# Optimization experiments

Hardware: AMD Instinct MI355X
Metric: run time of the kernel (lower is better)

Reference implementation:

```python
import jax, jax.numpy as jnp
import numpy as np

N_HEADS = 8
D_EMBED = 64
B, S = 2, 2048
ROPE_BASE = 10000.0


def apply_rope(x):
    # x: [b, h, s, d]; interleaved-pair rotary embedding over the s axis
    d = x.shape[-1]
    s = x.shape[-2]
    inv_freq = 1.0 / (ROPE_BASE ** (jnp.arange(0, d, 2, dtype=jnp.float32) / d))  # [d/2]
    angles = jnp.arange(s, dtype=jnp.float32)[:, None] * inv_freq[None, :]  # [s, d/2]
    cos = jnp.cos(angles)[None, None, :, :]
    sin = jnp.sin(angles)[None, None, :, :]
    x1 = x[..., 0::2]
    x2 = x[..., 1::2]
    out = jnp.stack([x1 * cos - x2 * sin, x1 * sin + x2 * cos], axis=-1)
    return out.reshape(x.shape)


def setup_inputs() -> dict:
    key = jax.random.key(0)
    ks = jax.random.split(key, 7)
    scale = 1.0 / np.sqrt(D_EMBED)
    return {
        "q": jax.random.normal(ks[0], (B, S, D_EMBED), dtype=jnp.float32),
        "k": jax.random.normal(ks[1], (B, S, D_EMBED), dtype=jnp.float32),
        "v": jax.random.normal(ks[2], (B, S, D_EMBED), dtype=jnp.float32),
        "W_q": jax.random.normal(ks[3], (N_HEADS, D_EMBED, D_EMBED), dtype=jnp.float32) * scale,
        "W_k": jax.random.normal(ks[4], (N_HEADS, D_EMBED, D_EMBED), dtype=jnp.float32) * scale,
        "W_v": jax.random.normal(ks[5], (N_HEADS, D_EMBED, D_EMBED), dtype=jnp.float32) * scale,
        "W_o": jax.random.normal(ks[6], (N_HEADS * D_EMBED, D_EMBED), dtype=jnp.float32) * scale,
    }


def reference(q, k, v, W_q, W_k, W_v, W_o):
    Bn, Sn, E = q.shape
    H = W_q.shape[0]
    qh = jnp.einsum('bsz,hzd->bhsd', q, W_q)
    kh = jnp.einsum('bsz,hzd->bhsd', k, W_k)
    vh = jnp.einsum('bsz,hzd->bhsd', v, W_v)
    qh = apply_rope(qh)
    kh = apply_rope(kh)
    attn_scaling = 1.0 / E  # note: 1/d, not 1/sqrt(d), per original
    scores = jnp.einsum('bhqd,bhkd->bhqk', qh, kh)
    causal = jnp.triu(jnp.ones((Sn, Sn), dtype=bool), k=1)
    scores = jnp.where(causal[None, None], -jnp.inf, scores) * attn_scaling
    probs = jax.nn.softmax(scores, axis=-1)
    # post-softmax diagonal zeroing (breaks normalization; this is the ICL twist)
    diag_mask = 1.0 - jnp.eye(Sn, dtype=probs.dtype)
    probs = probs * diag_mask[None, None]
    # NOTE: einsum 'bhzs,bhzd->bhsd' in the original contracts over the QUERY axis
    # (probs transposed): out[k-pos] = sum_q P[q, k-pos] * v[q]
    out = jnp.einsum('bhqk,bhqd->bhkd', probs, vh)
    out = out.transpose(0, 2, 1, 3).reshape(Bn, Sn, H * E)
    return jnp.einsum('bsz,zd->bsd', out, W_o)
```

## Files before the change

kernel.cpp:

```cpp
#include <hip/hip_runtime.h>
#include <math.h>

#define NH 8
#define D 64
#define BB 2
#define SS 2048
#define NBH (BB*NH)
#define LOG2E 1.4426950408889634f
#define NPAR 4

typedef short bf16x8 __attribute__((ext_vector_type(8)));
typedef float f32x4 __attribute__((ext_vector_type(4)));

#define MFMA16(a,b,c) __builtin_amdgcn_mfma_f32_16x16x32_bf16((a),(b),(c),0,0,0)

__device__ inline short f2bf(float f) {
    unsigned u = __float_as_uint(f);
    unsigned r = (u + 0x7fffu + ((u >> 16) & 1u)) >> 16;
    return (short)r;
}

__global__ __launch_bounds__(256) void wtrans_kernel(
    const float* __restrict__ Wq, const float* __restrict__ Wk,
    const float* __restrict__ Wv, const float* __restrict__ Wo,
    short* __restrict__ WqT, short* __restrict__ WkT, short* __restrict__ WvT,
    short* __restrict__ WoT) {
    int blk = blockIdx.x;
    int t = threadIdx.x;
    if (blk < 24) {
        int tensor = blk >> 3, h = blk & 7;
        const float* W = tensor == 0 ? Wq : (tensor == 1 ? Wk : Wv);
        short* WT = tensor == 0 ? WqT : (tensor == 1 ? WkT : WvT);
        __shared__ float wl[64][65];
        {
            int z = t >> 2, c0 = (t & 3) * 16;
            const float* src = W + (size_t)h * 4096 + (size_t)z * 64 + c0;
#pragma unroll
            for (int i = 0; i < 16; ++i) wl[z][c0 + i] = src[i];
        }
        __syncthreads();
        {
            int d = t >> 2, z0 = (t & 3) * 16;
            short* dst = WT + ((size_t)h * 64 + d) * 64 + z0;
#pragma unroll
            for (int i = 0; i < 16; ++i) dst[i] = f2bf(wl[z0 + i][d]);
        }
    } else {
        int idx = (blk - 24) * 256 + t;
        int d = idx >> 6;
        int zc = (idx & 63) * 32;
#pragma unroll
        for (int j = 0; j < 32; ++j) {
            int z = zc + j;
            WoT[(size_t)d * 2048 + z] = f2bf(Wo[(size_t)(z & 511) * 64 + d]);
        }
    }
}

__global__ __launch_bounds__(256) void proj_mfma_kernel(
    const float* __restrict__ xq, const float* __restrict__ xk,
    const float* __restrict__ xv,
    const short* __restrict__ WqT, const short* __restrict__ WkT,
    const short* __restrict__ WvT,
    short* __restrict__ qh, short* __restrict__ kh, short* __restrict__ vhT) {
    int blk = blockIdx.x;
    int tensor = blk / (NBH * 32);
    int rem = blk - tensor * (NBH * 32);
    int st = rem & 31, bh = rem >> 5;
    int h = bh & 7, b = bh >> 3;
    const float* x = tensor == 0 ? xq : (tensor == 1 ? xk : xv);
    const short* WT = tensor == 0 ? WqT : (tensor == 1 ? WkT : WvT);

    int t = threadIdx.x, w = t >> 6, lane = t & 63;
    int l15 = lane & 15, lg = lane >> 4;

    __shared__ short vt[64 * 64];

    int sA = st * 64 + w * 16 + l15;
    const float* xr = x + ((size_t)b * SS + sA) * D + lg * 8;
    bf16x8 a0, a1;
#pragma unroll
    for (int j = 0; j < 8; ++j) a0[j] = f2bf(xr[j]);
#pragma unroll
    for (int j = 0; j < 8; ++j) a1[j] = f2bf(xr[32 + j]);

    bf16x8 bfr[4][2];
#pragma unroll
    for (int ds_ = 0; ds_ < 4; ++ds_) {
        int d = ds_ * 16 + l15;
        const short* wp = WT + ((size_t)h * 64 + d) * 64 + lg * 8;
        bfr[ds_][0] = *(const bf16x8*)(wp);
        bfr[ds_][1] = *(const bf16x8*)(wp + 32);
    }

    f32x4 c[4];
#pragma unroll
    for (int ds_ = 0; ds_ < 4; ++ds_) {
        f32x4 z = {0.f, 0.f, 0.f, 0.f};
        z = MFMA16(a0, bfr[ds_][0], z);
        z = MFMA16(a1, bfr[ds_][1], z);
        c[ds_] = z;
    }

    int sbase = st * 64 + w * 16 + lg * 4;
    if (tensor < 2) {
        short* dst = tensor == 0 ? qh : kh;
        float scale = tensor == 0 ? (1.0f / 64.0f) : 1.0f;
#pragma unroll
        for (int ds_ = 0; ds_ < 4; ++ds_) {
            int d = ds_ * 16 + l15;
            float invf = exp2f(-(float)(d & ~1) * (13.287712379549449f / 64.0f));
#pragma unroll
            for (int r = 0; r < 4; ++r) {
                float v = c[ds_][r];
                float pr = __shfl_xor(v, 1);
                float ang = (float)(sbase + r) * invf;
                float cs = cosf(ang), sn = sinf(ang);
                float o = (d & 1) ? (pr * sn + v * cs) : (v * cs - pr * sn);
                dst[((size_t)bh * SS + sbase + r) * D + d] = f2bf(o * scale);
            }
        }
    } else {
#pragma unroll
        for (int ds_ = 0; ds_ < 4; ++ds_) {
            int d = ds_ * 16 + l15;
#pragma unroll
            for (int r = 0; r < 4; ++r) {
                int sc = w * 16 + lg * 4 + r;
                vt[d * 64 + (sc ^ ((d & 7) << 3))] = f2bf(c[ds_][r]);
            }
        }
        __syncthreads();
#pragma unroll
        for (int pp = 0; pp < 2; ++pp) {
            int idx = pp * 256 + t;
            int d = idx >> 3, a = idx & 7;
            bf16x8 val = *(const bf16x8*)&vt[d * 64 + ((a ^ (d & 7)) << 3)];
            *(bf16x8*)&vhT[((size_t)bh * D + d) * SS + st * 64 + a * 8] = val;
        }
    }
}

__global__ __launch_bounds__(256, 4) void colstats_kernel(
    const short* __restrict__ qh, const short* __restrict__ kh,
    float* __restrict__ lpart) {
    int blk = blockIdx.x;
    int ph = blk & 3, p = (blk >> 2) & 7, bh = blk >> 5;
    int t = threadIdx.x, w = t >> 6, lane = t & 63;
    int l15 = lane & 15, lg = lane >> 4;
    int qt = (w & 1) ? ((w >> 1) ? (23 - p) : (31 - p))
                     : ((w >> 1) ? (p + 8) : p);

    bf16x8 qb[4][2];
#pragma unroll
    for (int qs = 0; qs < 4; ++qs) {
        const short* qp = qh + ((size_t)bh * SS + qt * 64 + qs * 16 + l15) * D + lg * 8;
        qb[qs][0] = *(const bf16x8*)qp;
        qb[qs][1] = *(const bf16x8*)(qp + 32);
    }

    const short* kbase = kh + (size_t)bh * SS * D;
    float lsum[4] = {0.f, 0.f, 0.f, 0.f};

    for (int kt = ph; kt <= qt; kt += NPAR) {
        bool diag = (kt == qt);
#pragma unroll
        for (int ks = 0; ks < 4; ++ks) {
            const short* kp = kbase + (size_t)(kt * 64 + ks * 16 + l15) * D + lg * 8;
            bf16x8 ka0 = *(const bf16x8*)kp;
            bf16x8 ka1 = *(const bf16x8*)(kp + 32);
            int kb = kt * 64 + ks * 16 + lg * 4;
#pragma unroll
            for (int qs = 0; qs < 4; ++qs) {
                f32x4 s = {0.f, 0.f, 0.f, 0.f};
                s = MFMA16(ka0, qb[qs][0], s);
                s = MFMA16(ka1, qb[qs][1], s);
                int qc = qt * 64 + qs * 16 + l15;
#pragma unroll
                for (int r = 0; r < 4; ++r) {
                    float e = (!diag || kb + r <= qc) ? exp2f(s[r] * LOG2E) : 0.f;
                    lsum[qs] += e;
                }
            }
        }
    }
#pragma unroll
    for (int qs = 0; qs < 4; ++qs) {
        lsum[qs] += __shfl_xor(lsum[qs], 16);
        lsum[qs] += __shfl_xor(lsum[qs], 32);
    }
    if (lane < 16) {
#pragma unroll
        for (int qs = 0; qs < 4; ++qs)
            lpart[((size_t)ph * NBH + bh) * SS + qt * 64 + qs * 16 + lane] = lsum[qs];
    }
}

__global__ __launch_bounds__(256) void merge_stats_kernel(
    const float* __restrict__ lpart, float* __restrict__ ilarr) {
    size_t idx = (size_t)blockIdx.x * 256 + threadIdx.x;
    const size_t STR = (size_t)NBH * SS;
    float l = lpart[idx] + lpart[STR + idx] + lpart[2 * STR + idx] + lpart[3 * STR + idx];
    ilarr[idx] = 1.0f / l;
}

__global__ __launch_bounds__(256, 4) void pv_kernel(
    const short* __restrict__ qh, const short* __restrict__ kh,
    const short* __restrict__ vhT,
    const float* __restrict__ ilarr,
    short* __restrict__ attc) {
    int blk = blockIdx.x;
    int ph = blk & 3, p = (blk >> 2) & 15, bh = blk >> 6;
    int h = bh & 7, b = bh >> 3;
    int t = threadIdx.x, w = t >> 6, lane = t & 63;
    int l15 = lane & 15, lg = lane >> 4;
    int kt = (w & 1) ? (31 - p) : p;
    int hf = w >> 1;
    int row0 = kt * 64 + hf * 32;

    __shared__ short pl[4][32 * 64];
    short* plw = pl[w];

    bf16x8 ka[2][2];
#pragma unroll
    for (int rg = 0; rg < 2; ++rg) {
        const short* kp = kh + ((size_t)bh * SS + row0 + rg * 16 + l15) * D + lg * 8;
        ka[rg][0] = *(const bf16x8*)kp;
        ka[rg][1] = *(const bf16x8*)(kp + 32);
    }

    f32x4 acc[2][4];
#pragma unroll
    for (int rg = 0; rg < 2; ++rg)
#pragma unroll
        for (int i = 0; i < 4; ++i) acc[rg][i] = (f32x4){0.f, 0.f, 0.f, 0.f};

    int myk0 = row0 + lg * 4;
    const float* irow = ilarr + (size_t)bh * SS;
    const short* qbase = qh + (size_t)bh * SS * D;
    const short* vbase = vhT + (size_t)bh * D * SS;

    int qt0 = kt + ((ph - kt) & 3);
    for (int qt = qt0; qt < 32; qt += NPAR) {
        bool diag = (qt == kt);
        bf16x8 qb[4][2];
#pragma unroll
        for (int qs = 0; qs < 4; ++qs) {
            const short* qp2 = qbase + (size_t)(qt * 64 + qs * 16 + l15) * D + lg * 8;
            qb[qs][0] = *(const bf16x8*)qp2;
            qb[qs][1] = *(const bf16x8*)(qp2 + 32);
        }
#pragma unroll
        for (int qs = 0; qs < 4; ++qs) {
            int qrow = qs * 16 + l15;
            int qq = qt * 64 + qrow;
            float iq = irow[qq];
            f32x4 s0 = {0.f, 0.f, 0.f, 0.f};
            s0 = MFMA16(ka[0][0], qb[qs][0], s0);
            s0 = MFMA16(ka[0][1], qb[qs][1], s0);
            f32x4 s1 = {0.f, 0.f, 0.f, 0.f};
            s1 = MFMA16(ka[1][0], qb[qs][0], s1);
            s1 = MFMA16(ka[1][1], qb[qs][1], s1);
#pragma unroll
            for (int r = 0; r < 4; ++r) {
                float p0 = exp2f(s0[r] * LOG2E) * iq;
                float p1 = exp2f(s1[r] * LOG2E) * iq;
                if (diag && qq <= myk0 + r) p0 = 0.f;
                if (diag && qq <= myk0 + 16 + r) p1 = 0.f;
                int pr0 = lg * 4 + r;
                int pr1 = 16 + lg * 4 + r;
                plw[pr0 * 64 + (qrow ^ ((pr0 & 7) << 3))] = f2bf(p0);
                plw[pr1 * 64 + (qrow ^ ((pr1 & 7) << 3))] = f2bf(p1);
            }
        }
#pragma unroll
        for (int qhh = 0; qhh < 2; ++qhh) {
            int chunk = (qhh << 2) | lg;
            bf16x8 pa0 = *(const bf16x8*)&plw[l15 * 64 + ((chunk ^ (l15 & 7)) << 3)];
            bf16x8 pa1 = *(const bf16x8*)&plw[(16 + l15) * 64 + ((chunk ^ (l15 & 7)) << 3)];
#pragma unroll
            for (int ds_ = 0; ds_ < 4; ++ds_) {
                const short* vp2 = vbase + (size_t)(ds_ * 16 + l15) * SS + qt * 64 + chunk * 8;
                bf16x8 vb = *(const bf16x8*)vp2;
                acc[0][ds_] = MFMA16(pa0, vb, acc[0][ds_]);
                acc[1][ds_] = MFMA16(pa1, vb, acc[1][ds_]);
            }
        }
    }
#pragma unroll
    for (int rg = 0; rg < 2; ++rg)
#pragma unroll
        for (int ds_ = 0; ds_ < 4; ++ds_) {
            int d = ds_ * 16 + l15;
#pragma unroll
            for (int r = 0; r < 4; ++r) {
                int k = row0 + rg * 16 + lg * 4 + r;
                attc[((size_t)b * SS + k) * 2048 + ph * 512 + h * 64 + d] =
                    f2bf(acc[rg][ds_][r]);
            }
        }
}

__global__ __launch_bounds__(256) void outproj_kernel(
    const short* __restrict__ attc, const short* __restrict__ WoT,
    float* __restrict__ out) {
    int blk = blockIdx.x;
    int t = threadIdx.x, w = t >> 6, lane = t & 63;
    int l15 = lane & 15, lg = lane >> 4;
    int srow = blk * 16 + l15;
    const short* arow = attc + (size_t)srow * 2048 + lg * 8;

    f32x4 acc[4];
#pragma unroll
    for (int i = 0; i < 4; ++i) acc[i] = (f32x4){0.f, 0.f, 0.f, 0.f};

#pragma unroll
    for (int i = 0; i < 16; ++i) {
        int kc = w * 16 + i;
        bf16x8 af = *(const bf16x8*)(arow + kc * 32);
#pragma unroll
        for (int ds_ = 0; ds_ < 4; ++ds_) {
            bf16x8 bf_ = *(const bf16x8*)&WoT[(size_t)(ds_ * 16 + l15) * 2048 + kc * 32 + lg * 8];
            acc[ds_] = MFMA16(af, bf_, acc[ds_]);
        }
    }
    __shared__ float red[4][16 * 64];
#pragma unroll
    for (int ds_ = 0; ds_ < 4; ++ds_)
#pragma unroll
        for (int r = 0; r < 4; ++r)
            red[w][(lg * 4 + r) * 64 + ds_ * 16 + l15] = acc[ds_][r];
    __syncthreads();
    {
        int idx4 = t * 4;
        int row = idx4 >> 6, col = idx4 & 63;
        float4 s0 = *(const float4*)&red[0][row * 64 + col];
        float4 s1 = *(const float4*)&red[1][row * 64 + col];
        float4 s2 = *(const float4*)&red[2][row * 64 + col];
        float4 s3 = *(const float4*)&red[3][row * 64 + col];
        float4 sum;
        sum.x = s0.x + s1.x + s2.x + s3.x;
        sum.y = s0.y + s1.y + s2.y + s3.y;
        sum.z = s0.z + s1.z + s2.z + s3.z;
        sum.w = s0.w + s1.w + s2.w + s3.w;
        *(float4*)&out[(size_t)(blk * 16 + row) * 64 + col] = sum;
    }
}

extern "C" void kernel_launch(void* const* d_in, const int* in_sizes, int n_in,
                              void* d_out, int out_size, void* d_ws, size_t ws_size,
                              hipStream_t stream) {
    const float* q  = (const float*)d_in[0];
    const float* k  = (const float*)d_in[1];
    const float* v  = (const float*)d_in[2];
    const float* Wq = (const float*)d_in[3];
    const float* Wk = (const float*)d_in[4];
    const float* Wv = (const float*)d_in[5];
    const float* Wo = (const float*)d_in[6];
    float* out = (float*)d_out;

    const size_t PROJ = (size_t)NBH * SS * D;

    short* qh  = (short*)d_ws;
    short* kh  = qh + PROJ;
    short* vhT = kh + PROJ;
    short* WqT = vhT + PROJ;
    short* WkT = WqT + 32768;
    short* WvT = WkT + 32768;
    short* WoT = WvT + 32768;
    float* lpart = (float*)(WoT + 131072);
    float* ilarr = lpart + 4 * (size_t)NBH * SS;
    short* attc  = (short*)(ilarr + (size_t)NBH * SS);

    wtrans_kernel<<<40, 256, 0, stream>>>(Wq, Wk, Wv, Wo, WqT, WkT, WvT, WoT);

    proj_mfma_kernel<<<3 * NBH * 32, 256, 0, stream>>>(q, k, v, WqT, WkT, WvT,
                                                       qh, kh, vhT);

    colstats_kernel<<<NBH * 32, 256, 0, stream>>>(qh, kh, lpart);

    merge_stats_kernel<<<(NBH * SS) / 256, 256, 0, stream>>>(lpart, ilarr);

    pv_kernel<<<NBH * 64, 256, 0, stream>>>(qh, kh, vhT, ilarr, attc);

    outproj_kernel<<<256, 256, 0, stream>>>(attc, WoT, out);
}
```

Before: 112.0 us.

## Double attention split factor, fold 1/l normalization into V, use fast trig

Raises the split count over query tiles from four to eight in both the column-statistics and PV kernels, remapping block/wave indices so each block handles one tile with several partial splits. The per-query normalizer is folded into V with a new scale_v kernel rather than being multiplied into every probability inside the PV loop. Partial outputs are widened to eight slices, so the output projection's K dimension and the W_o transpose double. RoPE uses fast __sinf/__cosf. This adds parallelism and removes per-element multiplies, at the cost of an extra kernel, more partial-buffer traffic, and a larger out-projection reduction.

New measurement: 228.9 us. +104.5%, slower.

```diff
diff --git a/kernel.cpp b/kernel.cpp
--- a/kernel.cpp
+++ b/kernel.cpp
@@ -7,7 +7,7 @@
 #define SS 2048
 #define NBH (BB*NH)
 #define LOG2E 1.4426950408889634f
-#define NPAR 4
+#define NPAR 8
 
 typedef short bf16x8 __attribute__((ext_vector_type(8)));
 typedef float f32x4 __attribute__((ext_vector_type(4)));
@@ -18,6 +18,9 @@
     unsigned u = __float_as_uint(f);
     unsigned r = (u + 0x7fffu + ((u >> 16) & 1u)) >> 16;
     return (short)r;
+}
+__device__ inline float bf2f(short s) {
+    return __uint_as_float(((unsigned)(unsigned short)s) << 16);
 }
 
 __global__ __launch_bounds__(256) void wtrans_kernel(
@@ -47,12 +50,12 @@
         }
     } else {
         int idx = (blk - 24) * 256 + t;
-        int d = idx >> 6;
-        int zc = (idx & 63) * 32;
+        int d = idx >> 7;
+        int zc = (idx & 127) * 32;
 #pragma unroll
         for (int j = 0; j < 32; ++j) {
             int z = zc + j;
-            WoT[(size_t)d * 2048 + z] = f2bf(Wo[(size_t)(z & 511) * 64 + d]);
+            WoT[(size_t)d * 4096 + z] = f2bf(Wo[(size_t)(z & 511) * 64 + d]);
         }
     }
 }
@@ -115,7 +118,7 @@
                 float v = c[ds_][r];
                 float pr = __shfl_xor(v, 1);
                 float ang = (float)(sbase + r) * invf;
-                float cs = cosf(ang), sn = sinf(ang);
+                float cs = __cosf(ang), sn = __sinf(ang);
                 float o = (d & 1) ? (pr * sn + v * cs) : (v * cs - pr * sn);
                 dst[((size_t)bh * SS + sbase + r) * D + d] = f2bf(o * scale);
             }
@@ -145,11 +148,10 @@
     const short* __restrict__ qh, const short* __restrict__ kh,
     float* __restrict__ lpart) {
     int blk = blockIdx.x;
-    int ph = blk & 3, p = (blk >> 2) & 7, bh = blk >> 5;
+    int ph2 = blk & 1, qt = (blk >> 1) & 31, bh = blk >> 6;
     int t = threadIdx.x, w = t >> 6, lane = t & 63;
     int l15 = lane & 15, lg = lane >> 4;
-    int qt = (w & 1) ? ((w >> 1) ? (23 - p) : (31 - p))
-                     : ((w >> 1) ? (p + 8) : p);
+    int pp = ph2 * 4 + w;
 
     bf16x8 qb[4][2];
 #pragma unroll
@@ -162,7 +164,7 @@
     const short* kbase = kh + (size_t)bh * SS * D;
     float lsum[4] = {0.f, 0.f, 0.f, 0.f};
 
-    for (int kt = ph; kt <= qt; kt += NPAR) {
+    for (int kt = pp; kt <= qt; kt += NPAR) {
         bool diag = (kt == qt);
 #pragma unroll
         for (int ks = 0; ks < 4; ++ks) {
@@ -192,7 +194,7 @@
     if (lane < 16) {
 #pragma unroll
         for (int qs = 0; qs < 4; ++qs)
-            lpart[((size_t)ph * NBH + bh) * SS + qt * 64 + qs * 16 + lane] = lsum[qs];
+            lpart[((size_t)pp * NBH + bh) * SS + qt * 64 + qs * 16 + lane] = lsum[qs];
     }
 }
 
@@ -200,22 +202,37 @@
     const float* __restrict__ lpart, float* __restrict__ ilarr) {
     size_t idx = (size_t)blockIdx.x * 256 + threadIdx.x;
     const size_t STR = (size_t)NBH * SS;
-    float l = lpart[idx] + lpart[STR + idx] + lpart[2 * STR + idx] + lpart[3 * STR + idx];
+    float l = 0.f;
+#pragma unroll
+    for (int i = 0; i < NPAR; ++i) l += lpart[i * STR + idx];
     ilarr[idx] = 1.0f / l;
 }
 
-__global__ __launch_bounds__(256, 4) void pv_kernel(
+__global__ __launch_bounds__(256) void scale_v_kernel(
+    short* __restrict__ vhT, const float* __restrict__ ilarr) {
+    int idx = blockIdx.x * 256 + threadIdx.x;
+    int row = idx >> 8;
+    int chunk = idx & 255;
+    int bh = row >> 6;
+    size_t base = (size_t)row * SS + chunk * 8;
+    const float* il = ilarr + (size_t)bh * SS + chunk * 8;
+    bf16x8 v = *(bf16x8*)&vhT[base];
+#pragma unroll
+    for (int j = 0; j < 8; ++j) v[j] = f2bf(bf2f(v[j]) * il[j]);
+    *(bf16x8*)&vhT[base] = v;
+}
+
+__global__ __launch_bounds__(256, 8) void pv_kernel(
     const short* __restrict__ qh, const short* __restrict__ kh,
     const short* __restrict__ vhT,
-    const float* __restrict__ ilarr,
     short* __restrict__ attc) {
     int blk = blockIdx.x;
-    int ph = blk & 3, p = (blk >> 2) & 15, bh = blk >> 6;
+    int phb = blk & 3, kt = (blk >> 2) & 31, bh = blk >> 7;
     int h = bh & 7, b = bh >> 3;
     int t = threadIdx.x, w = t >> 6, lane = t & 63;
     int l15 = lane & 15, lg = lane >> 4;
-    int kt = (w & 1) ? (31 - p) : p;
-    int hf = w >> 1;
+    int hf = w >> 1, sp = w & 1;
+    int ph = phb * 2 + sp;
     int row0 = kt * 64 + hf * 32;
 
     __shared__ short pl[4][32 * 64];
@@ -236,11 +253,10 @@
         for (int i = 0; i < 4; ++i) acc[rg][i] = (f32x4){0.f, 0.f, 0.f, 0.f};
 
     int myk0 = row0 + lg * 4;
-    const float* irow = ilarr + (size_t)bh * SS;
     const short* qbase = qh + (size_t)bh * SS * D;
     const short* vbase = vhT + (size_t)bh * D * SS;
 
-    int qt0 = kt + ((ph - kt) & 3);
+    int qt0 = kt + ((ph - kt) & (NPAR - 1));
     for (int qt = qt0; qt < 32; qt += NPAR) {
         bool diag = (qt == kt);
         bf16x8 qb[4][2];
@@ -254,7 +270,6 @@
         for (int qs = 0; qs < 4; ++qs) {
             int qrow = qs * 16 + l15;
             int qq = qt * 64 + qrow;
-            float iq = irow[qq];
             f32x4 s0 = {0.f, 0.f, 0.f, 0.f};
             s0 = MFMA16(ka[0][0], qb[qs][0], s0);
             s0 = MFMA16(ka[0][1], qb[qs][1], s0);
@@ -263,8 +278,8 @@
             s1 = MFMA16(ka[1][1], qb[qs][1], s1);
 #pragma unroll
             for (int r = 0; r < 4; ++r) {
-                float p0 = exp2f(s0[r] * LOG2E) * iq;
-                float p1 = exp2f(s1[r] * LOG2E) * iq;
+                float p0 = exp2f(s0[r] * LOG2E);
+                float p1 = exp2f(s1[r] * LOG2E);
                 if (diag && qq <= myk0 + r) p0 = 0.f;
                 if (diag && qq <= myk0 + 16 + r) p1 = 0.f;
                 int pr0 = lg * 4 + r;
@@ -295,7 +310,7 @@
 #pragma unroll
             for (int r = 0; r < 4; ++r) {
                 int k = row0 + rg * 16 + lg * 4 + r;
-                attc[((size_t)b * SS + k) * 2048 + ph * 512 + h * 64 + d] =
+                attc[((size_t)b * SS + k) * 4096 + ph * 512 + h * 64 + d] =
                     f2bf(acc[rg][ds_][r]);
             }
         }
@@ -308,19 +323,19 @@
     int t = threadIdx.x, w = t >> 6, lane = t & 63;
     int l15 = lane & 15, lg = lane >> 4;
     int srow = blk * 16 + l15;
-    const short* arow = attc + (size_t)srow * 2048 + lg * 8;
+    const short* arow = attc + (size_t)srow * 4096 + lg * 8;
 
     f32x4 acc[4];
 #pragma unroll
     for (int i = 0; i < 4; ++i) acc[i] = (f32x4){0.f, 0.f, 0.f, 0.f};
 
 #pragma unroll
-    for (int i = 0; i < 16; ++i) {
-        int kc = w * 16 + i;
+    for (int i = 0; i < 32; ++i) {
+        int kc = w * 32 + i;
         bf16x8 af = *(const bf16x8*)(arow + kc * 32);
 #pragma unroll
         for (int ds_ = 0; ds_ < 4; ++ds_) {
-            bf16x8 bf_ = *(const bf16x8*)&WoT[(size_t)(ds_ * 16 + l15) * 2048 + kc * 32 + lg * 8];
+            bf16x8 bf_ = *(const bf16x8*)&WoT[(size_t)(ds_ * 16 + l15) * 4096 + kc * 32 + lg * 8];
             acc[ds_] = MFMA16(af, bf_, acc[ds_]);
         }
     }
@@ -368,20 +383,22 @@
     short* WkT = WqT + 32768;
     short* WvT = WkT + 32768;
     short* WoT = WvT + 32768;
-    float* lpart = (float*)(WoT + 131072);
-    float* ilarr = lpart + 4 * (size_t)NBH * SS;
+    float* lpart = (float*)(WoT + 262144);
+    float* ilarr = lpart + (size_t)NPAR * NBH * SS;
     short* attc  = (short*)(ilarr + (size_t)NBH * SS);
 
-    wtrans_kernel<<<40, 256, 0, stream>>>(Wq, Wk, Wv, Wo, WqT, WkT, WvT, WoT);
+    wtrans_kernel<<<56, 256, 0, stream>>>(Wq, Wk, Wv, Wo, WqT, WkT, WvT, WoT);
 
     proj_mfma_kernel<<<3 * NBH * 32, 256, 0, stream>>>(q, k, v, WqT, WkT, WvT,
                                                        qh, kh, vhT);
 
-    colstats_kernel<<<NBH * 32, 256, 0, stream>>>(qh, kh, lpart);
+    colstats_kernel<<<NBH * 64, 256, 0, stream>>>(qh, kh, lpart);
 
     merge_stats_kernel<<<(NBH * SS) / 256, 256, 0, stream>>>(lpart, ilarr);
 
-    pv_kernel<<<NBH * 64, 256, 0, stream>>>(qh, kh, vhT, ilarr, attc);
+    scale_v_kernel<<<(NBH * D * SS / 8) / 256, 256, 0, stream>>>(vhT, ilarr);
+
+    pv_kernel<<<NBH * 128, 256, 0, stream>>>(qh, kh, vhT, attc);
 
     outproj_kernel<<<256, 256, 0, stream>>>(attc, WoT, out);
 }
```

## Fold softmax normalizer into V and log2e into Q, rebalance colstats split

Applied to the files above, without the earlier changes.

Folds LOG2E into the Q projection scale so both the stats and PV kernels call exp2f directly without a multiply. The per-query inverse row sum is now applied to V (transposed, indexed by query) in a merge kernel, so the PV inner loop no longer loads or multiplies by the normalizer. Colstats switches to one query tile per block with 8-way key-tile partitioning across waves and blocks, for better load balance. PV computes Q·K with operands swapped so each lane writes packed 4-bf16 stores to LDS, and RoPE uses fast __sinf/__cosf. Risks are an extra bf16 rounding of V*il and reduced accuracy from the fast trig on large angles.

After: 103.5 us. 1.08x faster.

```diff
diff --git a/kernel.cpp b/kernel.cpp
--- a/kernel.cpp
+++ b/kernel.cpp
@@ -1,4 +1,5 @@
 #include <hip/hip_runtime.h>
+#include <hip/hip_bf16.h>
 #include <math.h>
 
 #define NH 8
@@ -7,7 +8,8 @@
 #define SS 2048
 #define NBH (BB*NH)
 #define LOG2E 1.4426950408889634f
-#define NPAR 4
+#define KPAR 8
+#define QPAR 4
 
 typedef short bf16x8 __attribute__((ext_vector_type(8)));
 typedef float f32x4 __attribute__((ext_vector_type(4)));
@@ -18,6 +20,15 @@
     unsigned u = __float_as_uint(f);
     unsigned r = (u + 0x7fffu + ((u >> 16) & 1u)) >> 16;
     return (short)r;
+}
+__device__ inline float bf2f(short s) {
+    return __uint_as_float(((unsigned)(unsigned short)s) << 16);
+}
+__device__ inline unsigned pack2bf(float a, float b) {
+    __hip_bfloat162 hv = __float22bfloat162_rn(make_float2(a, b));
+    unsigned u;
+    __builtin_memcpy(&u, &hv, 4);
+    return u;
 }
 
 __global__ __launch_bounds__(256) void wtrans_kernel(
@@ -105,7 +116,7 @@
     int sbase = st * 64 + w * 16 + lg * 4;
     if (tensor < 2) {
         short* dst = tensor == 0 ? qh : kh;
-        float scale = tensor == 0 ? (1.0f / 64.0f) : 1.0f;
+        float scale = tensor == 0 ? (LOG2E / 64.0f) : 1.0f;
 #pragma unroll
         for (int ds_ = 0; ds_ < 4; ++ds_) {
             int d = ds_ * 16 + l15;
@@ -115,7 +126,7 @@
                 float v = c[ds_][r];
                 float pr = __shfl_xor(v, 1);
                 float ang = (float)(sbase + r) * invf;
-                float cs = cosf(ang), sn = sinf(ang);
+                float cs = __cosf(ang), sn = __sinf(ang);
                 float o = (d & 1) ? (pr * sn + v * cs) : (v * cs - pr * sn);
                 dst[((size_t)bh * SS + sbase + r) * D + d] = f2bf(o * scale);
             }
@@ -145,11 +156,10 @@
     const short* __restrict__ qh, const short* __restrict__ kh,
     float* __restrict__ lpart) {
     int blk = blockIdx.x;
-    int ph = blk & 3, p = (blk >> 2) & 7, bh = blk >> 5;
+    int ph2 = blk & 1, qt = (blk >> 1) & 31, bh = blk >> 6;
     int t = threadIdx.x, w = t >> 6, lane = t & 63;
     int l15 = lane & 15, lg = lane >> 4;
-    int qt = (w & 1) ? ((w >> 1) ? (23 - p) : (31 - p))
-                     : ((w >> 1) ? (p + 8) : p);
+    int pp = ph2 * 4 + w;
 
     bf16x8 qb[4][2];
 #pragma unroll
@@ -162,7 +172,7 @@
     const short* kbase = kh + (size_t)bh * SS * D;
     float lsum[4] = {0.f, 0.f, 0.f, 0.f};
 
-    for (int kt = ph; kt <= qt; kt += NPAR) {
+    for (int kt = pp; kt <= qt; kt += KPAR) {
         bool diag = (kt == qt);
 #pragma unroll
         for (int ks = 0; ks < 4; ++ks) {
@@ -178,7 +188,7 @@
                 int qc = qt * 64 + qs * 16 + l15;
 #pragma unroll
                 for (int r = 0; r < 4; ++r) {
-                    float e = (!diag || kb + r <= qc) ? exp2f(s[r] * LOG2E) : 0.f;
+                    float e = (!diag || kb + r <= qc) ? exp2f(s[r]) : 0.f;
                     lsum[qs] += e;
                 }
             }
@@ -192,22 +202,40 @@
     if (lane < 16) {
 #pragma unroll
         for (int qs = 0; qs < 4; ++qs)
-            lpart[((size_t)ph * NBH + bh) * SS + qt * 64 + qs * 16 + lane] = lsum[qs];
-    }
-}
-
-__global__ __launch_bounds__(256) void merge_stats_kernel(
-    const float* __restrict__ lpart, float* __restrict__ ilarr) {
-    size_t idx = (size_t)blockIdx.x * 256 + threadIdx.x;
+            lpart[((size_t)pp * NBH + bh) * SS + qt * 64 + qs * 16 + lane] = lsum[qs];
+    }
+}
+
+__global__ __launch_bounds__(256) void merge_scale_kernel(
+    const float* __restrict__ lpart, short* __restrict__ vhT) {
+    int blk = blockIdx.x;
+    int qc = blk & 15, bh = blk >> 4;
+    int t = threadIdx.x;
     const size_t STR = (size_t)NBH * SS;
-    float l = lpart[idx] + lpart[STR + idx] + lpart[2 * STR + idx] + lpart[3 * STR + idx];
-    ilarr[idx] = 1.0f / l;
+    __shared__ float il[128];
+    if (t < 128) {
+        size_t idx = (size_t)bh * SS + qc * 128 + t;
+        float l = 0.f;
+#pragma unroll
+        for (int pp = 0; pp < KPAR; ++pp) l += lpart[pp * STR + idx];
+        il[t] = 1.0f / l;
+    }
+    __syncthreads();
+    int d = t >> 2, sub = t & 3;
+    size_t base = ((size_t)bh * 64 + d) * SS + qc * 128 + sub * 32;
+#pragma unroll
+    for (int j = 0; j < 32; j += 8) {
+        bf16x8 v = *(bf16x8*)&vhT[base + j];
+#pragma unroll
+        for (int jj = 0; jj < 8; ++jj)
+            v[jj] = f2bf(bf2f(v[jj]) * il[sub * 32 + j + jj]);
+        *(bf16x8*)&vhT[base + j] = v;
+    }
 }
 
 __global__ __launch_bounds__(256, 4) void pv_kernel(
     const short* __restrict__ qh, const short* __restrict__ kh,
     const short* __restrict__ vhT,
-    const float* __restrict__ ilarr,
     short* __restrict__ attc) {
     int blk = blockIdx.x;
     int ph = blk & 3, p = (blk >> 2) & 15, bh = blk >> 6;
@@ -221,12 +249,12 @@
     __shared__ short pl[4][32 * 64];
     short* plw = pl[w];
 
-    bf16x8 ka[2][2];
-#pragma unroll
-    for (int rg = 0; rg < 2; ++rg) {
-        const short* kp = kh + ((size_t)bh * SS + row0 + rg * 16 + l15) * D + lg * 8;
-        ka[rg][0] = *(const bf16x8*)kp;
-        ka[rg][1] = *(const bf16x8*)(kp + 32);
+    bf16x8 kb[2][2];
+#pragma unroll
+    for (int kg = 0; kg < 2; ++kg) {
+        const short* kp = kh + ((size_t)bh * SS + row0 + kg * 16 + l15) * D + lg * 8;
+        kb[kg][0] = *(const bf16x8*)kp;
+        kb[kg][1] = *(const bf16x8*)(kp + 32);
     }
 
     f32x4 acc[2][4];
@@ -235,49 +263,54 @@
 #pragma unroll
         for (int i = 0; i < 4; ++i) acc[rg][i] = (f32x4){0.f, 0.f, 0.f, 0.f};
 
-    int myk0 = row0 + lg * 4;
-    const float* irow = ilarr + (size_t)bh * SS;
     const short* qbase = qh + (size_t)bh * SS * D;
     const short* vbase = vhT + (size_t)bh * D * SS;
 
-    int qt0 = kt + ((ph - kt) & 3);
-    for (int qt = qt0; qt < 32; qt += NPAR) {
+    int qt0 = kt + ((ph - kt) & (QPAR - 1));
+    for (int qt = qt0; qt < 32; qt += QPAR) {
         bool diag = (qt == kt);
-        bf16x8 qb[4][2];
-#pragma unroll
-        for (int qs = 0; qs < 4; ++qs) {
-            const short* qp2 = qbase + (size_t)(qt * 64 + qs * 16 + l15) * D + lg * 8;
-            qb[qs][0] = *(const bf16x8*)qp2;
-            qb[qs][1] = *(const bf16x8*)(qp2 + 32);
-        }
-#pragma unroll
-        for (int qs = 0; qs < 4; ++qs) {
-            int qrow = qs * 16 + l15;
-            int qq = qt * 64 + qrow;
-            float iq = irow[qq];
-            f32x4 s0 = {0.f, 0.f, 0.f, 0.f};
-            s0 = MFMA16(ka[0][0], qb[qs][0], s0);
-            s0 = MFMA16(ka[0][1], qb[qs][1], s0);
-            f32x4 s1 = {0.f, 0.f, 0.f, 0.f};
-            s1 = MFMA16(ka[1][0], qb[qs][0], s1);
-            s1 = MFMA16(ka[1][1], qb[qs][1], s1);
-#pragma unroll
-            for (int r = 0; r < 4; ++r) {
-                float p0 = exp2f(s0[r] * LOG2E) * iq;
-                float p1 = exp2f(s1[r] * LOG2E) * iq;
-                if (diag && qq <= myk0 + r) p0 = 0.f;
-                if (diag && qq <= myk0 + 16 + r) p1 = 0.f;
-                int pr0 = lg * 4 + r;
-                int pr1 = 16 + lg * 4 + r;
-                plw[pr0 * 64 + (qrow ^ ((pr0 & 7) << 3))] = f2bf(p0);
-                plw[pr1 * 64 + (qrow ^ ((pr1 & 7) << 3))] = f2bf(p1);
+        bf16x8 qa[4][2];
+#pragma unroll
+        for (int qg = 0; qg < 4; ++qg) {
+            const short* qp2 = qbase + (size_t)(qt * 64 + qg * 16 + l15) * D + lg * 8;
+            qa[qg][0] = *(const bf16x8*)qp2;
+            qa[qg][1] = *(const bf16x8*)(qp2 + 32);
+        }
+#pragma unroll
+        for (int qg = 0; qg < 4; ++qg) {
+#pragma unroll
+            for (int kg = 0; kg < 2; ++kg) {
+                f32x4 s = {0.f, 0.f, 0.f, 0.f};
+                s = MFMA16(qa[qg][0], kb[kg][0], s);
+                s = MFMA16(qa[qg][1], kb[kg][1], s);
+                float p0 = exp2f(s[0]);
+                float p1 = exp2f(s[1]);
+                float p2 = exp2f(s[2]);
+                float p3 = exp2f(s[3]);
+                if (diag) {
+                    int qoff = qg * 16 + 4 * lg;
+                    int kk = hf * 32 + kg * 16 + l15;
+                    if (qoff + 0 <= kk) p0 = 0.f;
+                    if (qoff + 1 <= kk) p1 = 0.f;
+                    if (qoff + 2 <= kk) p2 = 0.f;
+                    if (qoff + 3 <= kk) p3 = 0.f;
+                }
+                unsigned u0 = pack2bf(p0, p1);
+                unsigned u1 = pack2bf(p2, p3);
+                int row = kg * 16 + l15;
+                int col = (qg * 16 + 4 * lg) ^ ((row & 7) << 3);
+                uint2 val;
+                val.x = u0;
+                val.y = u1;
+                *(uint2*)&plw[row * 64 + col] = val;
             }
         }
 #pragma unroll
         for (int qhh = 0; qhh < 2; ++qhh) {
             int chunk = (qhh << 2) | lg;
-            bf16x8 pa0 = *(const bf16x8*)&plw[l15 * 64 + ((chunk ^ (l15 & 7)) << 3)];
-            bf16x8 pa1 = *(const bf16x8*)&plw[(16 + l15) * 64 + ((chunk ^ (l15 & 7)) << 3)];
+            int cc = (chunk ^ (l15 & 7)) << 3;
+            bf16x8 pa0 = *(const bf16x8*)&plw[l15 * 64 + cc];
+            bf16x8 pa1 = *(const bf16x8*)&plw[(16 + l15) * 64 + cc];
 #pragma unroll
             for (int ds_ = 0; ds_ < 4; ++ds_) {
                 const short* vp2 = vbase + (size_t)(ds_ * 16 + l15) * SS + qt * 64 + chunk * 8;
@@ -369,19 +402,18 @@
     short* WvT = WkT + 32768;
     short* WoT = WvT + 32768;
     float* lpart = (float*)(WoT + 131072);
-    float* ilarr = lpart + 4 * (size_t)NBH * SS;
-    short* attc  = (short*)(ilarr + (size_t)NBH * SS);
+    short* attc  = (short*)(lpart + (size_t)KPAR * NBH * SS);
 
     wtrans_kernel<<<40, 256, 0, stream>>>(Wq, Wk, Wv, Wo, WqT, WkT, WvT, WoT);
 
     proj_mfma_kernel<<<3 * NBH * 32, 256, 0, stream>>>(q, k, v, WqT, WkT, WvT,
                                                        qh, kh, vhT);
 
-    colstats_kernel<<<NBH * 32, 256, 0, stream>>>(qh, kh, lpart);
-
-    merge_stats_kernel<<<(NBH * SS) / 256, 256, 0, stream>>>(lpart, ilarr);
-
-    pv_kernel<<<NBH * 64, 256, 0, stream>>>(qh, kh, vhT, ilarr, attc);
+    colstats_kernel<<<NBH * 64, 256, 0, stream>>>(qh, kh, lpart);
+
+    merge_scale_kernel<<<NBH * 16, 256, 0, stream>>>(lpart, vhT);
+
+    pv_kernel<<<NBH * 64, 256, 0, stream>>>(qh, kh, vhT, attc);
 
     outproj_kernel<<<256, 256, 0, stream>>>(attc, WoT, out);
 }
```
